# Performance work log

Measured on AMD Instinct MI355X. Metric: run time of the kernel, lower is better.

The kernel has to match this reference:

```python
import jax, jax.numpy as jnp
import numpy as np

B, S, H, D = 256, 512, 256, 512  # batch, n_seq, n_hid, n_dim
LN_EPS = 1e-5


def _xavier(key, fan_out, fan_in):
    lim = (6.0 / (fan_in + fan_out)) ** 0.5
    return jax.random.uniform(key, (fan_out, fan_in), jnp.float32, -lim, lim)


def setup_inputs() -> dict:
    key = jax.random.key(0)
    ks = jax.random.split(key, 10)
    x = jax.random.normal(ks[0], (B, S, D), jnp.float32)
    k_w = _xavier(ks[1], H, D)
    q_w = _xavier(ks[2], H, D)
    v_w = _xavier(ks[3], H, D)
    lb = 1.0 / (D ** 0.5)
    k_b = jax.random.uniform(ks[4], (H,), jnp.float32, -lb, lb)
    q_b = jax.random.uniform(ks[5], (H,), jnp.float32, -lb, lb)
    v_b = jax.random.uniform(ks[6], (H,), jnp.float32, -lb, lb)
    attn_bias = jax.random.normal(ks[7], (S, H), jnp.float32)
    ln_g = jnp.ones((H,), jnp.float32)
    ln_b = jnp.zeros((H,), jnp.float32)
    lo = 1.0 / ((S * H) ** 0.5)
    out_w = jax.random.uniform(ks[8], (D, S * H), jnp.float32, -lo, lo)
    out_b = jax.random.uniform(ks[9], (D,), jnp.float32, -lo, lo)
    return {"x": x, "k_w": k_w, "k_b": k_b, "q_w": q_w, "q_b": q_b,
            "v_w": v_w, "v_b": v_b, "attn_bias": attn_bias,
            "ln_g": ln_g, "ln_b": ln_b, "out_w": out_w, "out_b": out_b}


def reference(x, k_w, k_b, q_w, q_b, v_w, v_b, attn_bias, ln_g, ln_b, out_w, out_b):
    # projections: [B,S,D] -> [B,S,H]
    k = jnp.einsum('bsd,hd->bsh', x, k_w) + k_b
    q = jnp.einsum('bsd,hd->bsh', x, q_w) + q_b
    v = jnp.einsum('bsd,hd->bsh', x, v_w) + v_b
    # scores = k^T q, scaled by BATCH size^-0.5 (faithful to v.shape[0]**-0.5)
    scale = x.shape[0] ** (-0.5)
    scores = jnp.einsum('bsh,bsg->bhg', k, q) * scale  # [B,H,H]
    weight = jax.nn.softmax(scores, axis=1)
    out = jnp.einsum('bsh,bhg->bsg', v, weight)  # [B,S,H]
    out = out + attn_bias
    # LayerNorm over last dim
    mu = out.mean(-1, keepdims=True)
    var = out.var(-1, keepdims=True)
    out = (out - mu) * jax.lax.rsqrt(var + LN_EPS) * ln_g + ln_b
    # dropout is identity in eval mode; exact (erf) GELU matches torch default
    out = jax.nn.gelu(out, approximate=False)
    out = out.reshape(out.shape[0], S * H)
    out = out @ out_w.T + out_b  # [B,D]
    return out[:, None, :]  # [B,1,D]
```

## Files before the change

kernel.cpp:

```cpp
#include <hip/hip_runtime.h>
#include <hip/hip_bf16.h>
#include <math.h>

#define B_ 256
#define S_ 512
#define H_ 256
#define D_ 512

typedef __bf16 bf16;
typedef __bf16 bf16x8 __attribute__((ext_vector_type(8)));
typedef float  f32x4  __attribute__((ext_vector_type(4)));
typedef unsigned short u16x8 __attribute__((ext_vector_type(8)));
typedef unsigned short u16x4 __attribute__((ext_vector_type(4)));

#define MFMA(a, b, c) __builtin_amdgcn_mfma_f32_16x16x32_bf16((a), (b), (c), 0, 0, 0)

__device__ __forceinline__ int swz(int row, int kbyte) {
  return (row * 128 + kbyte) ^ ((row & 7) << 4);
}
__device__ __forceinline__ unsigned short bfbits(float f) {
  bf16 h = (bf16)f;
  union { bf16 b; unsigned short u; } c; c.b = h; return c.u;
}
__device__ __forceinline__ bf16x8 cvt8(const float* __restrict__ p) {
  f32x4 a = *(const f32x4*)p;
  f32x4 b = *(const f32x4*)(p + 4);
  bf16x8 r;
  r[0] = (bf16)a[0]; r[1] = (bf16)a[1]; r[2] = (bf16)a[2]; r[3] = (bf16)a[3];
  r[4] = (bf16)b[0]; r[5] = (bf16)b[1]; r[6] = (bf16)b[2]; r[7] = (bf16)b[3];
  return r;
}
__device__ __forceinline__ void gload16(const unsigned short* g, unsigned char* l) {
  __builtin_amdgcn_global_load_lds(
      (const __attribute__((address_space(1))) unsigned int*)g,
      (__attribute__((address_space(3))) unsigned int*)l, 16, 0, 0);
}

__global__ __launch_bounds__(256) void k_convw(
    const float* __restrict__ kw, const float* __restrict__ qw,
    const float* __restrict__ vw, unsigned short* __restrict__ wc)
{
  const int r = blockIdx.x;
  const float* src = (r < 256) ? kw + (size_t)r * 512
                   : (r < 512) ? qw + (size_t)(r - 256) * 512
                               : vw + (size_t)(r - 512) * 512;
#pragma unroll
  for (int q = 0; q < 2; ++q) {
    const int c = threadIdx.x * 2 + q;
    const int sc = (c & ~63) | (((((c >> 3) & 7) ^ (r & 7))) << 3) | (c & 7);
    wc[(size_t)r * 512 + c] = bfbits(src[sc]);
  }
}

__global__ __launch_bounds__(256, 2) void k_proj6(
    const float* __restrict__ x,
    const unsigned short* __restrict__ wc,
    const float* __restrict__ kbi, const float* __restrict__ qbi,
    const float* __restrict__ vbi,
    unsigned short* __restrict__ k_t, unsigned short* __restrict__ q_t,
    unsigned short* __restrict__ v_o, int nwg)
{
  __shared__ __align__(16) unsigned char sA[32768];
  __shared__ __align__(16) unsigned char sB[32768];

  const int o = blockIdx.x;
  const int cpx = nwg >> 3;
  const int a = (o & 7) * cpx + (o >> 3);
  const int mt = a / 3;
  const int region = a - mt * 3;
  const int m0 = mt * 128;
  const int w0 = region * 256;
  const float* __restrict__ Bi = (region == 0) ? kbi : (region == 1) ? qbi : vbi;

  const int tid = threadIdx.x;
  const int lane = tid & 63;
  const int wid = tid >> 6;
  const int wm = wid >> 1;
  const int wn = wid & 1;
  const int l15 = lane & 15;
  const int l16 = lane >> 4;
  const int lr8 = lane >> 3;
  const int lk8 = (lane & 7) << 3;
  const int ar4 = lane >> 4;
  const int aslot = l15;

  f32x4 acc[4][8];
#pragma unroll
  for (int i = 0; i < 4; ++i)
#pragma unroll
    for (int j = 0; j < 8; ++j) acc[i][j] = (f32x4){0.f, 0.f, 0.f, 0.f};

  for (int kt = 0; kt < 8; ++kt) {
    if (kt) __syncthreads();
#pragma unroll
    for (int i = 0; i < 8; ++i) {
      const int chunk = wid * 8 + i;
      const int arow = chunk * 4 + ar4;
      const int gslot = aslot ^ (arow & 7);
      gload16((const unsigned short*)(
                  x + (size_t)(m0 + arow) * D_ + kt * 64 + gslot * 4),
              sA + chunk * 1024);
    }
#pragma unroll
    for (int i = 0; i < 8; ++i) {
      const int chunk = wid * 8 + i;
      const int row = chunk * 8 + lr8;
      gload16(wc + (size_t)(w0 + row) * 512 + kt * 64 + lk8, sB + chunk * 1024);
    }
    __syncthreads();
#pragma unroll
    for (int ks = 0; ks < 2; ++ks) {
      const int kb2 = ks * 64 + (l16 << 4);
      const int sbase = ks * 8 + l16 * 2;
      bf16x8 av[4], bv[8];
#pragma unroll
      for (int f = 0; f < 4; ++f) {
        const int row = wm * 64 + f * 16 + l15;
        const int sw = row & 7;
        const unsigned char* pr = sA + row * 256;
        f32x4 lo = *(const f32x4*)(pr + ((sbase ^ sw) << 4));
        f32x4 hi = *(const f32x4*)(pr + (((sbase + 1) ^ sw) << 4));
        bf16x8 r;
        r[0] = (bf16)lo[0]; r[1] = (bf16)lo[1];
        r[2] = (bf16)lo[2]; r[3] = (bf16)lo[3];
        r[4] = (bf16)hi[0]; r[5] = (bf16)hi[1];
        r[6] = (bf16)hi[2]; r[7] = (bf16)hi[3];
        av[f] = r;
      }
#pragma unroll
      for (int f = 0; f < 8; ++f)
        bv[f] = *(const bf16x8*)(sB + swz(wn * 128 + f * 16 + l15, kb2));
#pragma unroll
      for (int fm = 0; fm < 4; ++fm)
#pragma unroll
        for (int fn = 0; fn < 8; ++fn)
          acc[fm][fn] = MFMA(av[fm], bv[fn], acc[fm][fn]);
    }
  }

  const int b = m0 >> 9;
  const int sbase = m0 & 511;
  const int r4 = l16 * 4;
#pragma unroll
  for (int fn = 0; fn < 8; ++fn) {
    const int hcol = wn * 128 + fn * 16 + l15;
    const float bias = Bi[hcol];
#pragma unroll
    for (int fm = 0; fm < 4; ++fm) {
      const int s = sbase + wm * 64 + fm * 16 + r4;
      if (region < 2) {
        unsigned short* dst = ((region == 0) ? k_t : q_t) +
                              (size_t)b * (H_ * S_) + (size_t)hcol * S_ + s;
        u16x4 ov;
#pragma unroll
        for (int j = 0; j < 4; ++j) ov[j] = bfbits(acc[fm][fn][j] + bias);
        *(u16x4*)dst = ov;
      } else {
#pragma unroll
        for (int j = 0; j < 4; ++j)
          v_o[(size_t)b * (S_ * H_) + (size_t)(s + j) * H_ + hcol] =
              bfbits(acc[fm][fn][j] + bias);
      }
    }
  }
}

__global__ __launch_bounds__(1024, 4) void k_attn(
    const unsigned short* __restrict__ k_t,
    const unsigned short* __restrict__ q_t,
    const unsigned short* __restrict__ v_o,
    const float* __restrict__ attn_bias,
    const float* __restrict__ lng, const float* __restrict__ lnb,
    unsigned short* __restrict__ act)
{
  __shared__ __align__(16) unsigned char sm[163840];
  unsigned char* sP = sm;
  float* redm = (float*)(sm + 131072);
  float* reds = (float*)(sm + 131072 + 4096);
  float* lbuf = (float*)(sm + 147456);

  const int tid = threadIdx.x;
  const int lane = tid & 63;
  const int wid = tid >> 6;
  const int l15 = lane & 15;
  const int l16 = lane >> 4;
  const int b = blockIdx.x;
  const int wh = wid >> 2;
  const int wq = wid & 3;

  const unsigned short* __restrict__ Kb = k_t + (size_t)b * (H_ * S_);
  const unsigned short* __restrict__ Qb = q_t + (size_t)b * (H_ * S_);
  const unsigned short* __restrict__ Vb = v_o + (size_t)b * (S_ * H_);

  const int srow8 = lane >> 3;
  const int scol16 = (lane & 7) ^ srow8;

  auto stage1 = [&](int t, int buf) {
#pragma unroll
    for (int i = 0; i < 2; ++i) {
      const int cb = wid * 2 + i;
      const int row = cb * 8 + srow8;
      gload16(Kb + (size_t)row * S_ + t * 64 + scol16 * 8,
              sm + buf * 65536 + cb * 1024);
      gload16(Qb + (size_t)row * S_ + t * 64 + scol16 * 8,
              sm + buf * 65536 + 32768 + cb * 1024);
    }
  };

  f32x4 acc1[4][4];
#pragma unroll
  for (int i = 0; i < 4; ++i)
#pragma unroll
    for (int j = 0; j < 4; ++j) acc1[i][j] = (f32x4){0.f, 0.f, 0.f, 0.f};

  stage1(0, 0);
  for (int t = 0; t < 8; ++t) {
    const int cur = t & 1;
    if (t < 7) stage1(t + 1, cur ^ 1);
    if (t < 7) asm volatile("s_waitcnt vmcnt(4)" ::: "memory");
    else       asm volatile("s_waitcnt vmcnt(0)" ::: "memory");
    __builtin_amdgcn_s_barrier();
    __builtin_amdgcn_sched_barrier(0);
    const unsigned char* sK = sm + cur * 65536;
    const unsigned char* sQ = sK + 32768;
#pragma unroll
    for (int ks = 0; ks < 2; ++ks) {
      const int kb2 = ks * 64 + l16 * 16;
      bf16x8 av[4], bv[4];
#pragma unroll
      for (int f = 0; f < 4; ++f)
        av[f] = *(const bf16x8*)(sK + swz(wh * 64 + f * 16 + l15, kb2));
#pragma unroll
      for (int f = 0; f < 4; ++f)
        bv[f] = *(const bf16x8*)(sQ + swz(wq * 64 + f * 16 + l15, kb2));
#pragma unroll
      for (int fm = 0; fm < 4; ++fm)
#pragma unroll
        for (int fn = 0; fn < 4; ++fn)
          acc1[fm][fn] = MFMA(av[fm], bv[fn], acc1[fm][fn]);
    }
    __builtin_amdgcn_sched_barrier(0);
    __builtin_amdgcn_s_barrier();
  }

  float cmax[4] = {-3.0e38f, -3.0e38f, -3.0e38f, -3.0e38f};
#pragma unroll
  for (int fm = 0; fm < 4; ++fm)
#pragma unroll
    for (int fn = 0; fn < 4; ++fn)
#pragma unroll
      for (int j = 0; j < 4; ++j) {
        acc1[fm][fn][j] *= 0.0625f;
        cmax[fn] = fmaxf(cmax[fn], acc1[fm][fn][j]);
      }
#pragma unroll
  for (int fn = 0; fn < 4; ++fn) {
    cmax[fn] = fmaxf(cmax[fn], __shfl_xor(cmax[fn], 16));
    cmax[fn] = fmaxf(cmax[fn], __shfl_xor(cmax[fn], 32));
  }
  if (lane < 16) {
#pragma unroll
    for (int fn = 0; fn < 4; ++fn)
      redm[wh * 256 + wq * 64 + fn * 16 + lane] = cmax[fn];
  }
  __syncthreads();
  float gmax[4];
#pragma unroll
  for (int fn = 0; fn < 4; ++fn) {
    const int c = wq * 64 + fn * 16 + l15;
    gmax[fn] = fmaxf(fmaxf(redm[c], redm[256 + c]),
                     fmaxf(redm[512 + c], redm[768 + c]));
  }
  float csum[4] = {0.f, 0.f, 0.f, 0.f};
#pragma unroll
  for (int fm = 0; fm < 4; ++fm)
#pragma unroll
    for (int fn = 0; fn < 4; ++fn)
#pragma unroll
      for (int j = 0; j < 4; ++j) {
        float p = __expf(acc1[fm][fn][j] - gmax[fn]);
        acc1[fm][fn][j] = p;
        csum[fn] += p;
      }
#pragma unroll
  for (int fn = 0; fn < 4; ++fn) {
    csum[fn] += __shfl_xor(csum[fn], 16);
    csum[fn] += __shfl_xor(csum[fn], 32);
  }
  if (lane < 16) {
#pragma unroll
    for (int fn = 0; fn < 4; ++fn)
      reds[wh * 256 + wq * 64 + fn * 16 + lane] = csum[fn];
  }
  __syncthreads();
  float gi[4];
#pragma unroll
  for (int fn = 0; fn < 4; ++fn) {
    const int c = wq * 64 + fn * 16 + l15;
    gi[fn] = 1.0f / (reds[c] + reds[256 + c] + reds[512 + c] + reds[768 + c]);
  }

#pragma unroll
  for (int fn = 0; fn < 4; ++fn) {
    const int g = wq * 64 + fn * 16 + l15;
#pragma unroll
    for (int fm = 0; fm < 4; ++fm) {
      const int h0 = wh * 64 + fm * 16 + l16 * 4;
      u16x4 pv;
#pragma unroll
      for (int j = 0; j < 4; ++j) pv[j] = bfbits(acc1[fm][fn][j] * gi[fn]);
      *(u16x4*)(sP + ((g * 512 + h0 * 2) ^ ((g & 7) << 4))) = pv;
    }
  }
  __syncthreads();

  const int vrow = tid >> 2;
  const int vcol16 = (tid & 3) ^ ((vrow >> 1) & 3);

  auto stageV = [&](int t) {
    const int so_ = t >> 3, kh_ = t & 7;
    gload16(Vb + (size_t)(so_ * 256 + vrow) * H_ + kh_ * 32 + vcol16 * 8,
            sm + 131072 + (t & 1) * 16384 + wid * 1024);
  };

  f32x4 acc2[4][4];
  stageV(0);
  for (int t = 0; t < 16; ++t) {
    const int so = t >> 3, kh = t & 7, cur = t & 1;
    if (kh == 0) {
#pragma unroll
      for (int i = 0; i < 4; ++i)
#pragma unroll
        for (int j = 0; j < 4; ++j) acc2[i][j] = (f32x4){0.f, 0.f, 0.f, 0.f};
    }
    if (t < 15) stageV(t + 1);
    if (t < 15) asm volatile("s_waitcnt vmcnt(1)" ::: "memory");
    else        asm volatile("s_waitcnt vmcnt(0)" ::: "memory");
    __builtin_amdgcn_s_barrier();
    __builtin_amdgcn_sched_barrier(0);
    const unsigned char* sV = sm + 131072 + cur * 16384;
    bf16x8 av[4], bv[4];
#pragma unroll
    for (int f = 0; f < 4; ++f) {
      const int rl = wh * 64 + f * 16 + l15;
      av[f] = *(const bf16x8*)(sV + rl * 64 + ((l16 ^ ((rl >> 1) & 3)) << 4));
    }
#pragma unroll
    for (int fn = 0; fn < 4; ++fn) {
      const int g = wq * 64 + fn * 16 + l15;
      bv[fn] = *(const bf16x8*)(
          sP + ((g * 512 + kh * 64 + l16 * 16) ^ ((g & 7) << 4)));
    }
#pragma unroll
    for (int f = 0; f < 4; ++f)
#pragma unroll
      for (int fn = 0; fn < 4; ++fn)
        acc2[f][fn] = MFMA(av[f], bv[fn], acc2[f][fn]);
    __builtin_amdgcn_sched_barrier(0);

    if (kh == 7) {
      __syncthreads();
#pragma unroll
      for (int f = 0; f < 4; ++f) {
#pragma unroll
        for (int j = 0; j < 4; ++j) {
          const int rloc = wh * 64 + f * 16 + l16 * 4 + j;
          const int s = so * 256 + rloc;
          float ps = 0.f, psq = 0.f;
#pragma unroll
          for (int fn = 0; fn < 4; ++fn) {
            const int g = wq * 64 + fn * 16 + l15;
            float vv = acc2[f][fn][j] + attn_bias[(size_t)s * H_ + g];
            acc2[f][fn][j] = vv;
            ps += vv; psq += vv * vv;
          }
          ps += __shfl_xor(ps, 1);  psq += __shfl_xor(psq, 1);
          ps += __shfl_xor(ps, 2);  psq += __shfl_xor(psq, 2);
          ps += __shfl_xor(ps, 4);  psq += __shfl_xor(psq, 4);
          ps += __shfl_xor(ps, 8);  psq += __shfl_xor(psq, 8);
          if (l15 == 0) {
            lbuf[wq * 256 + rloc] = ps;
            lbuf[1024 + wq * 256 + rloc] = psq;
          }
        }
      }
      __syncthreads();
#pragma unroll
      for (int f = 0; f < 4; ++f) {
#pragma unroll
        for (int j = 0; j < 4; ++j) {
          const int rloc = wh * 64 + f * 16 + l16 * 4 + j;
          const int s = so * 256 + rloc;
          float sum = lbuf[rloc] + lbuf[256 + rloc] +
                      lbuf[512 + rloc] + lbuf[768 + rloc];
          float sq  = lbuf[1024 + rloc] + lbuf[1280 + rloc] +
                      lbuf[1536 + rloc] + lbuf[1792 + rloc];
          float mu = sum * (1.f / H_);
          float var = sq * (1.f / H_) - mu * mu;
          float rstd = rsqrtf(var + 1e-5f);
#pragma unroll
          for (int fn = 0; fn < 4; ++fn) {
            const int g = wq * 64 + fn * 16 + l15;
            float xv = (acc2[f][fn][j] - mu) * rstd * lng[g] + lnb[g];
            float y = 0.5f * xv * (1.f + erff(xv * 0.70710678118654752f));
            act[(size_t)b * (S_ * H_) + (size_t)s * H_ + g] = bfbits(y);
          }
        }
      }
      __syncthreads();
    } else {
      __builtin_amdgcn_s_barrier();
    }
  }
}

__global__ __launch_bounds__(512) void k_final(
    const unsigned short* __restrict__ act,
    const float* __restrict__ ow,
    float* __restrict__ partial)
{
  __shared__ __align__(16) unsigned char sA[256 * 128];
  __shared__ __align__(16) unsigned char sB[64 * 128];

  const int tid = threadIdx.x;
  const int lane = tid & 63;
  const int wid = tid >> 6;
  const int wm = wid >> 1;
  const int wn = wid & 1;
  const int n0 = blockIdx.x * 64;
  const size_t k0 = (size_t)blockIdx.y * 4096;

  f32x4 acc[4][2];
#pragma unroll
  for (int i = 0; i < 4; ++i)
#pragma unroll
    for (int j = 0; j < 2; ++j) acc[i][j] = (f32x4){0.f, 0.f, 0.f, 0.f};

  for (int kt = 0; kt < 64; ++kt) {
    const size_t kb = k0 + kt * 64;
    __syncthreads();
#pragma unroll
    for (int i = 0; i < 4; ++i) {
      int c = tid + i * 512;
      int row = c >> 3, kc = (c & 7) * 8;
      *(u16x8*)(sA + swz(row, kc * 2)) =
          *(const u16x8*)(act + (size_t)row * 131072 + kb + kc);
    }
    {
      int row = tid >> 3, kc = (tid & 7) * 8;
      *(bf16x8*)(sB + swz(row, kc * 2)) =
          cvt8(ow + (size_t)(n0 + row) * 131072 + kb + kc);
    }
    __syncthreads();
#pragma unroll
    for (int ks = 0; ks < 2; ++ks) {
      const int kbyte = ks * 64 + (lane >> 4) * 16;
      bf16x8 av[4], bv[2];
#pragma unroll
      for (int f = 0; f < 4; ++f)
        av[f] = *(const bf16x8*)(sA + swz(wm * 64 + f * 16 + (lane & 15), kbyte));
#pragma unroll
      for (int f = 0; f < 2; ++f)
        bv[f] = *(const bf16x8*)(sB + swz(wn * 32 + f * 16 + (lane & 15), kbyte));
#pragma unroll
      for (int fm = 0; fm < 4; ++fm)
#pragma unroll
        for (int fn = 0; fn < 2; ++fn)
          acc[fm][fn] = MFMA(av[fm], bv[fn], acc[fm][fn]);
    }
  }

  float* __restrict__ P = partial + (size_t)blockIdx.y * (256 * 512);
  const int r4 = (lane >> 4) * 4;
#pragma unroll
  for (int fn = 0; fn < 2; ++fn) {
    int col = n0 + wn * 32 + fn * 16 + (lane & 15);
#pragma unroll
    for (int fm = 0; fm < 4; ++fm) {
      int mb = wm * 64 + fm * 16 + r4;
#pragma unroll
      for (int j = 0; j < 4; ++j)
        P[(size_t)(mb + j) * 512 + col] = acc[fm][fn][j];
    }
  }
}

__global__ __launch_bounds__(256) void k_reduce(
    const float* __restrict__ partial,
    const float* __restrict__ ob,
    float* __restrict__ out)
{
  const int i4 = blockIdx.x * 256 + threadIdx.x;
  f32x4 s = *(const f32x4*)(ob + ((i4 & 127) << 2));
#pragma unroll
  for (int ks = 0; ks < 32; ++ks)
    s += *(const f32x4*)(partial + (size_t)ks * 131072 + (size_t)i4 * 4);
  *(f32x4*)(out + (size_t)i4 * 4) = s;
}

extern "C" void kernel_launch(void* const* d_in, const int* in_sizes, int n_in,
                              void* d_out, int out_size, void* d_ws, size_t ws_size,
                              hipStream_t stream) {
  const float* x         = (const float*)d_in[0];
  const float* k_w       = (const float*)d_in[1];
  const float* k_b       = (const float*)d_in[2];
  const float* q_w       = (const float*)d_in[3];
  const float* q_b       = (const float*)d_in[4];
  const float* v_w       = (const float*)d_in[5];
  const float* v_b       = (const float*)d_in[6];
  const float* attn_bias = (const float*)d_in[7];
  const float* ln_g      = (const float*)d_in[8];
  const float* ln_b      = (const float*)d_in[9];
  const float* out_w     = (const float*)d_in[10];
  const float* out_b     = (const float*)d_in[11];
  float* out = (float*)d_out;

  char* ws = (char*)d_ws;
  unsigned short* k_t = (unsigned short*)(ws);
  unsigned short* q_t = (unsigned short*)(ws + 67108864);
  unsigned short* v_o = (unsigned short*)(ws + 134217728);
  unsigned short* wc  = (unsigned short*)(ws + 201326592);
  unsigned short* act = k_t;
  float* partial      = (float*)(ws + 67108864);

  k_convw<<<dim3(768), dim3(256), 0, stream>>>(k_w, q_w, v_w, wc);

  const int nwg = 3072;
  k_proj6<<<dim3(nwg), dim3(256), 0, stream>>>(
      x, wc, k_b, q_b, v_b, k_t, q_t, v_o, nwg);

  k_attn<<<dim3(256), dim3(1024), 0, stream>>>(
      k_t, q_t, v_o, attn_bias, ln_g, ln_b, act);

  k_final<<<dim3(8, 32), dim3(512), 0, stream>>>(act, out_w, partial);
  k_reduce<<<dim3(128), dim3(256), 0, stream>>>(partial, out_b, out);
}
```

Before: 465.8 us.

## Split fused attention into separate scores-softmax and PV-LayerNorm kernels

The single per-batch attention kernel (one 1024-thread block per batch) is replaced by two kernels. The first computes scores and the column softmax for half of the output columns per block. It writes the bf16 weights back into the q_t workspace, overwriting exactly the Q rows that block already consumed. The second kernel computes V·W plus bias, LayerNorm and GELU for a quarter of the sequence per block. Both kernels use a batch-to-XCD block mapping to raise block count and occupancy. In exchange, the weights take an extra global round trip, K is loaded twice, and the double-buffered LDS pipelining is dropped.

Result: slower. 489.8 us (+5.2%).

```diff
diff --git a/kernel.cpp b/kernel.cpp
--- a/kernel.cpp
+++ b/kernel.cpp
@@ -165,64 +165,56 @@
   }
 }
 
-__global__ __launch_bounds__(1024, 4) void k_attn(
+__global__ __launch_bounds__(512, 4) void k_scores2(
     const unsigned short* __restrict__ k_t,
     const unsigned short* __restrict__ q_t,
-    const unsigned short* __restrict__ v_o,
-    const float* __restrict__ attn_bias,
-    const float* __restrict__ lng, const float* __restrict__ lnb,
-    unsigned short* __restrict__ act)
+    unsigned short* __restrict__ w_t)
 {
-  __shared__ __align__(16) unsigned char sm[163840];
-  unsigned char* sP = sm;
-  float* redm = (float*)(sm + 131072);
-  float* reds = (float*)(sm + 131072 + 4096);
-  float* lbuf = (float*)(sm + 147456);
+  __shared__ __align__(16) unsigned char sK[32768];
+  __shared__ __align__(16) unsigned char sQ[16384];
+  __shared__ float red[2][4][128];
+
+  const int o = blockIdx.x;
+  const int xcd = o & 7, t8 = o >> 3;
+  const int gh = t8 & 1;
+  const int b  = xcd * 32 + (t8 >> 1);
 
   const int tid = threadIdx.x;
   const int lane = tid & 63;
   const int wid = tid >> 6;
   const int l15 = lane & 15;
   const int l16 = lane >> 4;
-  const int b = blockIdx.x;
-  const int wh = wid >> 2;
-  const int wq = wid & 3;
+  const int wh = wid >> 1;
+  const int wg = wid & 1;
 
   const unsigned short* __restrict__ Kb = k_t + (size_t)b * (H_ * S_);
-  const unsigned short* __restrict__ Qb = q_t + (size_t)b * (H_ * S_);
-  const unsigned short* __restrict__ Vb = v_o + (size_t)b * (S_ * H_);
+  const unsigned short* __restrict__ Qb = q_t + (size_t)b * (H_ * S_) +
+                                          (size_t)(gh * 128) * S_;
 
   const int srow8 = lane >> 3;
   const int scol16 = (lane & 7) ^ srow8;
 
-  auto stage1 = [&](int t, int buf) {
+  f32x4 acc[4][4];
+#pragma unroll
+  for (int i = 0; i < 4; ++i)
+#pragma unroll
+    for (int j = 0; j < 4; ++j) acc[i][j] = (f32x4){0.f, 0.f, 0.f, 0.f};
+
+  for (int t = 0; t < 8; ++t) {
+    if (t) __syncthreads();
+#pragma unroll
+    for (int i = 0; i < 4; ++i) {
+      const int cb = wid * 4 + i;
+      const int row = cb * 8 + srow8;
+      gload16(Kb + (size_t)row * S_ + t * 64 + scol16 * 8, sK + cb * 1024);
+    }
 #pragma unroll
     for (int i = 0; i < 2; ++i) {
       const int cb = wid * 2 + i;
       const int row = cb * 8 + srow8;
-      gload16(Kb + (size_t)row * S_ + t * 64 + scol16 * 8,
-              sm + buf * 65536 + cb * 1024);
-      gload16(Qb + (size_t)row * S_ + t * 64 + scol16 * 8,
-              sm + buf * 65536 + 32768 + cb * 1024);
-    }
-  };
-
-  f32x4 acc1[4][4];
-#pragma unroll
-  for (int i = 0; i < 4; ++i)
-#pragma unroll
-    for (int j = 0; j < 4; ++j) acc1[i][j] = (f32x4){0.f, 0.f, 0.f, 0.f};
-
-  stage1(0, 0);
-  for (int t = 0; t < 8; ++t) {
-    const int cur = t & 1;
-    if (t < 7) stage1(t + 1, cur ^ 1);
-    if (t < 7) asm volatile("s_waitcnt vmcnt(4)" ::: "memory");
-    else       asm volatile("s_waitcnt vmcnt(0)" ::: "memory");
-    __builtin_amdgcn_s_barrier();
-    __builtin_amdgcn_sched_barrier(0);
-    const unsigned char* sK = sm + cur * 65536;
-    const unsigned char* sQ = sK + 32768;
+      gload16(Qb + (size_t)row * S_ + t * 64 + scol16 * 8, sQ + cb * 1024);
+    }
+    __syncthreads();
 #pragma unroll
     for (int ks = 0; ks < 2; ++ks) {
       const int kb2 = ks * 64 + l16 * 16;
@@ -232,15 +224,13 @@
         av[f] = *(const bf16x8*)(sK + swz(wh * 64 + f * 16 + l15, kb2));
 #pragma unroll
       for (int f = 0; f < 4; ++f)
-        bv[f] = *(const bf16x8*)(sQ + swz(wq * 64 + f * 16 + l15, kb2));
+        bv[f] = *(const bf16x8*)(sQ + swz(wg * 64 + f * 16 + l15, kb2));
 #pragma unroll
       for (int fm = 0; fm < 4; ++fm)
 #pragma unroll
         for (int fn = 0; fn < 4; ++fn)
-          acc1[fm][fn] = MFMA(av[fm], bv[fn], acc1[fm][fn]);
-    }
-    __builtin_amdgcn_sched_barrier(0);
-    __builtin_amdgcn_s_barrier();
+          acc[fm][fn] = MFMA(av[fm], bv[fn], acc[fm][fn]);
+    }
   }
 
   float cmax[4] = {-3.0e38f, -3.0e38f, -3.0e38f, -3.0e38f};
@@ -250,8 +240,8 @@
     for (int fn = 0; fn < 4; ++fn)
 #pragma unroll
       for (int j = 0; j < 4; ++j) {
-        acc1[fm][fn][j] *= 0.0625f;
-        cmax[fn] = fmaxf(cmax[fn], acc1[fm][fn][j]);
+        acc[fm][fn][j] *= 0.0625f;
+        cmax[fn] = fmaxf(cmax[fn], acc[fm][fn][j]);
       }
 #pragma unroll
   for (int fn = 0; fn < 4; ++fn) {
@@ -261,15 +251,15 @@
   if (lane < 16) {
 #pragma unroll
     for (int fn = 0; fn < 4; ++fn)
-      redm[wh * 256 + wq * 64 + fn * 16 + lane] = cmax[fn];
+      red[0][wh][wg * 64 + fn * 16 + lane] = cmax[fn];
   }
   __syncthreads();
   float gmax[4];
 #pragma unroll
   for (int fn = 0; fn < 4; ++fn) {
-    const int c = wq * 64 + fn * 16 + l15;
-    gmax[fn] = fmaxf(fmaxf(redm[c], redm[256 + c]),
-                     fmaxf(redm[512 + c], redm[768 + c]));
+    const int c = wg * 64 + fn * 16 + l15;
+    gmax[fn] = fmaxf(fmaxf(red[0][0][c], red[0][1][c]),
+                     fmaxf(red[0][2][c], red[0][3][c]));
   }
   float csum[4] = {0.f, 0.f, 0.f, 0.f};
 #pragma unroll
@@ -278,8 +268,8 @@
     for (int fn = 0; fn < 4; ++fn)
 #pragma unroll
       for (int j = 0; j < 4; ++j) {
-        float p = __expf(acc1[fm][fn][j] - gmax[fn]);
-        acc1[fm][fn][j] = p;
+        float p = __expf(acc[fm][fn][j] - gmax[fn]);
+        acc[fm][fn][j] = p;
         csum[fn] += p;
       }
 #pragma unroll
@@ -290,126 +280,145 @@
   if (lane < 16) {
 #pragma unroll
     for (int fn = 0; fn < 4; ++fn)
-      reds[wh * 256 + wq * 64 + fn * 16 + lane] = csum[fn];
+      red[1][wh][wg * 64 + fn * 16 + lane] = csum[fn];
   }
   __syncthreads();
   float gi[4];
 #pragma unroll
   for (int fn = 0; fn < 4; ++fn) {
-    const int c = wq * 64 + fn * 16 + l15;
-    gi[fn] = 1.0f / (reds[c] + reds[256 + c] + reds[512 + c] + reds[768 + c]);
-  }
-
+    const int c = wg * 64 + fn * 16 + l15;
+    gi[fn] = 1.0f / (red[1][0][c] + red[1][1][c] + red[1][2][c] + red[1][3][c]);
+  }
+
+  const size_t wbase = (size_t)b * 131072 + (size_t)gh * 65536;
 #pragma unroll
   for (int fn = 0; fn < 4; ++fn) {
-    const int g = wq * 64 + fn * 16 + l15;
+    const int g_loc = wg * 64 + fn * 16 + l15;
 #pragma unroll
     for (int fm = 0; fm < 4; ++fm) {
       const int h0 = wh * 64 + fm * 16 + l16 * 4;
-      u16x4 pv;
-#pragma unroll
-      for (int j = 0; j < 4; ++j) pv[j] = bfbits(acc1[fm][fn][j] * gi[fn]);
-      *(u16x4*)(sP + ((g * 512 + h0 * 2) ^ ((g & 7) << 4))) = pv;
+      u16x4 ov;
+#pragma unroll
+      for (int j = 0; j < 4; ++j) ov[j] = bfbits(acc[fm][fn][j] * gi[fn]);
+      *(u16x4*)(w_t + wbase + (size_t)g_loc * 256 + h0) = ov;
+    }
+  }
+}
+
+__global__ __launch_bounds__(512, 4) void k_pv2(
+    const unsigned short* __restrict__ v_o,
+    const unsigned short* __restrict__ w_t,
+    const float* __restrict__ attn_bias,
+    const float* __restrict__ lng, const float* __restrict__ lnb,
+    unsigned short* __restrict__ act)
+{
+  __shared__ __align__(16) unsigned char sV[16384];
+  __shared__ __align__(16) unsigned char sW[32768];
+  __shared__ float lbuf[2][4][128];
+
+  const int o = blockIdx.x;
+  const int xcd = o & 7, t8 = o >> 3;
+  const int sh = t8 & 3;
+  const int b  = xcd * 32 + (t8 >> 2);
+
+  const int tid = threadIdx.x;
+  const int lane = tid & 63;
+  const int wid = tid >> 6;
+  const int l15 = lane & 15;
+  const int l16 = lane >> 4;
+  const int ws2 = wid >> 2;
+  const int wgq = wid & 3;
+
+  const unsigned short* __restrict__ Vb = v_o + (size_t)b * (S_ * H_) +
+                                          (size_t)(sh * 128) * H_;
+  const unsigned short* __restrict__ Wb = w_t + (size_t)b * 131072;
+
+  const int srow8 = lane >> 3;
+  const int scol16 = (lane & 7) ^ srow8;
+
+  f32x4 acc[4][4];
+#pragma unroll
+  for (int i = 0; i < 4; ++i)
+#pragma unroll
+    for (int j = 0; j < 4; ++j) acc[i][j] = (f32x4){0.f, 0.f, 0.f, 0.f};
+
+  for (int kt = 0; kt < 4; ++kt) {
+    if (kt) __syncthreads();
+#pragma unroll
+    for (int i = 0; i < 2; ++i) {
+      const int cb = wid * 2 + i;
+      const int row = cb * 8 + srow8;
+      gload16(Vb + (size_t)row * H_ + kt * 64 + scol16 * 8, sV + cb * 1024);
+    }
+#pragma unroll
+    for (int i = 0; i < 4; ++i) {
+      const int cb = wid * 4 + i;
+      const int row = cb * 8 + srow8;
+      gload16(Wb + (size_t)(row >> 7) * 65536 + (size_t)(row & 127) * 256 +
+                  kt * 64 + scol16 * 8,
+              sW + cb * 1024);
+    }
+    __syncthreads();
+#pragma unroll
+    for (int ks = 0; ks < 2; ++ks) {
+      const int kb2 = ks * 64 + l16 * 16;
+      bf16x8 av[4], bv[4];
+#pragma unroll
+      for (int f = 0; f < 4; ++f)
+        av[f] = *(const bf16x8*)(sV + swz(ws2 * 64 + f * 16 + l15, kb2));
+#pragma unroll
+      for (int f = 0; f < 4; ++f)
+        bv[f] = *(const bf16x8*)(sW + swz(wgq * 64 + f * 16 + l15, kb2));
+#pragma unroll
+      for (int fm = 0; fm < 4; ++fm)
+#pragma unroll
+        for (int fn = 0; fn < 4; ++fn)
+          acc[fm][fn] = MFMA(av[fm], bv[fn], acc[fm][fn]);
+    }
+  }
+
+#pragma unroll
+  for (int fm = 0; fm < 4; ++fm) {
+#pragma unroll
+    for (int j = 0; j < 4; ++j) {
+      const int rloc = ws2 * 64 + fm * 16 + l16 * 4 + j;
+      const int s = sh * 128 + rloc;
+      float ps = 0.f, psq = 0.f;
+#pragma unroll
+      for (int fn = 0; fn < 4; ++fn) {
+        const int g = wgq * 64 + fn * 16 + l15;
+        float vv = acc[fm][fn][j] + attn_bias[(size_t)s * H_ + g];
+        acc[fm][fn][j] = vv;
+        ps += vv; psq += vv * vv;
+      }
+      ps += __shfl_xor(ps, 1);  psq += __shfl_xor(psq, 1);
+      ps += __shfl_xor(ps, 2);  psq += __shfl_xor(psq, 2);
+      ps += __shfl_xor(ps, 4);  psq += __shfl_xor(psq, 4);
+      ps += __shfl_xor(ps, 8);  psq += __shfl_xor(psq, 8);
+      if (l15 == 0) { lbuf[0][wgq][rloc] = ps; lbuf[1][wgq][rloc] = psq; }
     }
   }
   __syncthreads();
-
-  const int vrow = tid >> 2;
-  const int vcol16 = (tid & 3) ^ ((vrow >> 1) & 3);
-
-  auto stageV = [&](int t) {
-    const int so_ = t >> 3, kh_ = t & 7;
-    gload16(Vb + (size_t)(so_ * 256 + vrow) * H_ + kh_ * 32 + vcol16 * 8,
-            sm + 131072 + (t & 1) * 16384 + wid * 1024);
-  };
-
-  f32x4 acc2[4][4];
-  stageV(0);
-  for (int t = 0; t < 16; ++t) {
-    const int so = t >> 3, kh = t & 7, cur = t & 1;
-    if (kh == 0) {
-#pragma unroll
-      for (int i = 0; i < 4; ++i)
-#pragma unroll
-        for (int j = 0; j < 4; ++j) acc2[i][j] = (f32x4){0.f, 0.f, 0.f, 0.f};
-    }
-    if (t < 15) stageV(t + 1);
-    if (t < 15) asm volatile("s_waitcnt vmcnt(1)" ::: "memory");
-    else        asm volatile("s_waitcnt vmcnt(0)" ::: "memory");
-    __builtin_amdgcn_s_barrier();
-    __builtin_amdgcn_sched_barrier(0);
-    const unsigned char* sV = sm + 131072 + cur * 16384;
-    bf16x8 av[4], bv[4];
-#pragma unroll
-    for (int f = 0; f < 4; ++f) {
-      const int rl = wh * 64 + f * 16 + l15;
-      av[f] = *(const bf16x8*)(sV + rl * 64 + ((l16 ^ ((rl >> 1) & 3)) << 4));
-    }
-#pragma unroll
-    for (int fn = 0; fn < 4; ++fn) {
-      const int g = wq * 64 + fn * 16 + l15;
-      bv[fn] = *(const bf16x8*)(
-          sP + ((g * 512 + kh * 64 + l16 * 16) ^ ((g & 7) << 4)));
-    }
-#pragma unroll
-    for (int f = 0; f < 4; ++f)
-#pragma unroll
-      for (int fn = 0; fn < 4; ++fn)
-        acc2[f][fn] = MFMA(av[f], bv[fn], acc2[f][fn]);
-    __builtin_amdgcn_sched_barrier(0);
-
-    if (kh == 7) {
-      __syncthreads();
-#pragma unroll
-      for (int f = 0; f < 4; ++f) {
-#pragma unroll
-        for (int j = 0; j < 4; ++j) {
-          const int rloc = wh * 64 + f * 16 + l16 * 4 + j;
-          const int s = so * 256 + rloc;
-          float ps = 0.f, psq = 0.f;
-#pragma unroll
-          for (int fn = 0; fn < 4; ++fn) {
-            const int g = wq * 64 + fn * 16 + l15;
-            float vv = acc2[f][fn][j] + attn_bias[(size_t)s * H_ + g];
-            acc2[f][fn][j] = vv;
-            ps += vv; psq += vv * vv;
-          }
-          ps += __shfl_xor(ps, 1);  psq += __shfl_xor(psq, 1);
-          ps += __shfl_xor(ps, 2);  psq += __shfl_xor(psq, 2);
-          ps += __shfl_xor(ps, 4);  psq += __shfl_xor(psq, 4);
-          ps += __shfl_xor(ps, 8);  psq += __shfl_xor(psq, 8);
-          if (l15 == 0) {
-            lbuf[wq * 256 + rloc] = ps;
-            lbuf[1024 + wq * 256 + rloc] = psq;
-          }
-        }
+#pragma unroll
+  for (int fm = 0; fm < 4; ++fm) {
+#pragma unroll
+    for (int j = 0; j < 4; ++j) {
+      const int rloc = ws2 * 64 + fm * 16 + l16 * 4 + j;
+      const int s = sh * 128 + rloc;
+      float sum = lbuf[0][0][rloc] + lbuf[0][1][rloc] +
+                  lbuf[0][2][rloc] + lbuf[0][3][rloc];
+      float sq  = lbuf[1][0][rloc] + lbuf[1][1][rloc] +
+                  lbuf[1][2][rloc] + lbuf[1][3][rloc];
+      float mu = sum * (1.f / H_);
+      float var = sq * (1.f / H_) - mu * mu;
+      float rstd = rsqrtf(var + 1e-5f);
+#pragma unroll
+      for (int fn = 0; fn < 4; ++fn) {
+        const int g = wgq * 64 + fn * 16 + l15;
+        float xv = (acc[fm][fn][j] - mu) * rstd * lng[g] + lnb[g];
+        float y = 0.5f * xv * (1.f + erff(xv * 0.70710678118654752f));
+        act[(size_t)b * (S_ * H_) + (size_t)s * H_ + g] = bfbits(y);
       }
-      __syncthreads();
-#pragma unroll
-      for (int f = 0; f < 4; ++f) {
-#pragma unroll
-        for (int j = 0; j < 4; ++j) {
-          const int rloc = wh * 64 + f * 16 + l16 * 4 + j;
-          const int s = so * 256 + rloc;
-          float sum = lbuf[rloc] + lbuf[256 + rloc] +
-                      lbuf[512 + rloc] + lbuf[768 + rloc];
-          float sq  = lbuf[1024 + rloc] + lbuf[1280 + rloc] +
-                      lbuf[1536 + rloc] + lbuf[1792 + rloc];
-          float mu = sum * (1.f / H_);
-          float var = sq * (1.f / H_) - mu * mu;
-          float rstd = rsqrtf(var + 1e-5f);
-#pragma unroll
-          for (int fn = 0; fn < 4; ++fn) {
-            const int g = wq * 64 + fn * 16 + l15;
-            float xv = (acc2[f][fn][j] - mu) * rstd * lng[g] + lnb[g];
-            float y = 0.5f * xv * (1.f + erff(xv * 0.70710678118654752f));
-            act[(size_t)b * (S_ * H_) + (size_t)s * H_ + g] = bfbits(y);
-          }
-        }
-      }
-      __syncthreads();
-    } else {
-      __builtin_amdgcn_s_barrier();
     }
   }
 }
@@ -529,8 +538,9 @@
   k_proj6<<<dim3(nwg), dim3(256), 0, stream>>>(
       x, wc, k_b, q_b, v_b, k_t, q_t, v_o, nwg);
 
-  k_attn<<<dim3(256), dim3(1024), 0, stream>>>(
-      k_t, q_t, v_o, attn_bias, ln_g, ln_b, act);
+  k_scores2<<<dim3(512), dim3(512), 0, stream>>>(k_t, q_t, q_t);
+  k_pv2<<<dim3(1024), dim3(512), 0, stream>>>(
+      v_o, q_t, attn_bias, ln_g, ln_b, act);
 
   k_final<<<dim3(8, 32), dim3(512), 0, stream>>>(act, out_w, partial);
   k_reduce<<<dim3(128), dim3(256), 0, stream>>>(partial, out_b, out);
```
